# Performance work log

Hardware: AMD Instinct MI355X
Metric: run time of the kernel (lower is better)

The kernel has to match this reference:

```python
import jax, jax.numpy as jnp
import numpy as np


def _gcs_conv(x, a, w1, w2, b):
    # GCSConv: relu(A @ x W1 + x W2 + b);  x:[B,N,F], a:[B,N,N]
    return jax.nn.relu(jnp.einsum('bij,bjh->bih', a, x @ w1) + x @ w2 + b)


def _topk_pool(x, a, p, ratio=0.5):
    # score y = x . p/||p||, keep top ceil(ratio*N) nodes per graph,
    # gate kept node features with sigmoid(y), slice adjacency rows+cols.
    y = x @ (p / jnp.linalg.norm(p))            # [B, N]
    k = int(np.ceil(ratio * y.shape[1]))
    yk, idx = jax.lax.top_k(y, k)               # [B, k]
    xk = jnp.take_along_axis(x, idx[:, :, None], axis=1)
    xk = xk * jax.nn.sigmoid(yk)[:, :, None]    # gated node features [B,k,H]
    ak = jnp.take_along_axis(a, idx[:, :, None], axis=1)
    ak = jnp.take_along_axis(ak, idx[:, None, :], axis=2)  # [B,k,k]
    return xk, ak


def setup_inputs() -> dict:
    B, N, F0, H, C = 256, 512, 128, 32, 16
    key = jax.random.key(0)
    ks = jax.random.split(key, 12)
    s = lambda fan: 1.0 / np.sqrt(fan)
    return {
        'x': jax.random.normal(ks[0], (B, N, F0), jnp.float32),
        'a': jax.random.uniform(ks[1], (B, N, N), jnp.float32),
        'w1_1': jax.random.normal(ks[2], (F0, H), jnp.float32) * s(F0),
        'w2_1': jax.random.normal(ks[3], (F0, H), jnp.float32) * s(F0),
        'b1': jnp.zeros((H,), jnp.float32),
        'w1_2': jax.random.normal(ks[4], (H, H), jnp.float32) * s(H),
        'w2_2': jax.random.normal(ks[5], (H, H), jnp.float32) * s(H),
        'b2': jnp.zeros((H,), jnp.float32),
        'w1_3': jax.random.normal(ks[6], (H, H), jnp.float32) * s(H),
        'w2_3': jax.random.normal(ks[7], (H, H), jnp.float32) * s(H),
        'b3': jnp.zeros((H,), jnp.float32),
        'p_pool': jax.random.normal(ks[8], (H,), jnp.float32),
        'wd': jax.random.normal(ks[9], (H, C), jnp.float32) * s(H),
        'bd': jnp.zeros((C,), jnp.float32),
    }


def reference(x, a, w1_1, w2_1, b1, w1_2, w2_2, b2, w1_3, w2_3, b3, p_pool, wd, bd):
    x = _gcs_conv(x, a, w1_1, w2_1, b1)
    # NOTE: original code reuses pool1 twice -> shared p_pool for both stages
    x1, a1 = _topk_pool(x, a, p_pool)
    x1 = _gcs_conv(x1, a1, w1_2, w2_2, b2)
    x2, a2 = _topk_pool(x1, a1, p_pool)
    x2 = _gcs_conv(x2, a2, w1_3, w2_3, b3)
    pooled = jnp.mean(x2, axis=1)               # GlobalAvgPool over nodes [B,H]
    return jax.nn.softmax(pooled @ wd + bd, axis=-1)
```

## Files before the change

kernel.cpp:

```cpp
#include <hip/hip_runtime.h>
#include <cmath>

#define B 256
#define N0 512
#define F0 128
#define H 32
#define NC 16

template<int F, int RPT, int NPB, bool SCATTER>
__global__ __launch_bounds__(256) void k_xw(
    const float* __restrict__ x, const float* __restrict__ w1,
    const float* __restrict__ w2, const float* __restrict__ bias,
    const int* __restrict__ sidx,
    float* __restrict__ h, float* __restrict__ g) {
  __shared__ float w1t[H][F + 4];
  __shared__ float w2t[H][F + 4];
  __shared__ float bs[H];
  const int tid = threadIdx.x;
  for (int i = tid; i < F * H; i += 256) {
    int f = i >> 5, hc = i & 31;
    w1t[hc][f] = w1[i];
    w2t[hc][f] = w2[i];
  }
  if (tid < H) bs[tid] = bias[tid];
  __syncthreads();
  const int hq = tid & 7;
  const int rq = tid >> 3;
  const size_t row0 = (size_t)blockIdx.x * (32 * RPT) + (size_t)rq * RPT;
  const float* xb = x + row0 * F;
  float acc1[RPT][4];
  float acc2[RPT][4];
  #pragma unroll
  for (int r = 0; r < RPT; ++r)
    for (int c = 0; c < 4; ++c) { acc1[r][c] = 0.f; acc2[r][c] = 0.f; }
  for (int f0 = 0; f0 < F; f0 += 4) {
    float4 w1v[4], w2v[4];
    #pragma unroll
    for (int hh = 0; hh < 4; ++hh) {
      w1v[hh] = *(const float4*)&w1t[hq * 4 + hh][f0];
      w2v[hh] = *(const float4*)&w2t[hq * 4 + hh][f0];
    }
    #pragma unroll
    for (int r = 0; r < RPT; ++r) {
      float4 xv = *(const float4*)(xb + (size_t)r * F + f0);
      #pragma unroll
      for (int hh = 0; hh < 4; ++hh) {
        acc1[r][hh] += xv.x * w1v[hh].x + xv.y * w1v[hh].y + xv.z * w1v[hh].z + xv.w * w1v[hh].w;
        acc2[r][hh] += xv.x * w2v[hh].x + xv.y * w2v[hh].y + xv.z * w2v[hh].z + xv.w * w2v[hh].w;
      }
    }
  }
  #pragma unroll
  for (int r = 0; r < RPT; ++r) {
    size_t row = row0 + r;
    size_t go = row * H + hq * 4;
    size_t ho;
    if (SCATTER) {
      int b = (int)(row / NPB);
      int gid = sidx[row];
      ho = ((size_t)b * N0 + gid) * H + hq * 4;
    } else {
      ho = go;
    }
    float4 hv = make_float4(acc1[r][0], acc1[r][1], acc1[r][2], acc1[r][3]);
    float4 gv = make_float4(acc2[r][0] + bs[hq * 4 + 0], acc2[r][1] + bs[hq * 4 + 1],
                            acc2[r][2] + bs[hq * 4 + 2], acc2[r][3] + bs[hq * 4 + 3]);
    *(float4*)(h + ho) = hv;
    *(float4*)(g + go) = gv;
  }
}

template<int NROW, int RPT>
__global__ __launch_bounds__(256) void k_amm(
    const float* __restrict__ a0, const int* __restrict__ rid,
    const float* __restrict__ hf, const float* __restrict__ gbuf,
    float* __restrict__ out) {
  constexpr int RB = 32 * RPT;
  constexpr int JC = 64;
  constexpr int AS = JC + 2;
  __shared__ float atile[RB][AS];
  __shared__ float htile[JC][H];
  __shared__ int rowid[RB];
  const int tid = threadIdx.x;
  const int b = blockIdx.x;
  const int row0 = blockIdx.y * RB;
  for (int i = tid; i < RB; i += 256) {
    int row = row0 + i;
    rowid[i] = rid ? rid[(size_t)b * NROW + row] : row;
  }
  __syncthreads();
  const int hq = tid & 7;
  const int rq = tid >> 3;
  const float* abase = a0 + (size_t)b * N0 * N0;
  float acc[RPT][4];
  #pragma unroll
  for (int r = 0; r < RPT; ++r) { acc[r][0] = acc[r][1] = acc[r][2] = acc[r][3] = 0.f; }
  for (int j0 = 0; j0 < N0; j0 += JC) {
    if (j0) __syncthreads();
    {
      const float4* src = (const float4*)(hf + ((size_t)b * N0 + j0) * H);
      float4* dst = (float4*)htile;
      #pragma unroll
      for (int i = 0; i < JC * H / 4 / 256; ++i) dst[tid + i * 256] = src[tid + i * 256];
    }
    #pragma unroll
    for (int i = 0; i < RB * 16 / 256; ++i) {
      int c = tid + i * 256;
      int r = c >> 4, jc = c & 15;
      float4 v = *(const float4*)(abase + (size_t)rowid[r] * N0 + j0 + jc * 4);
      *(float2*)&atile[r][jc * 4] = make_float2(v.x, v.y);
      *(float2*)&atile[r][jc * 4 + 2] = make_float2(v.z, v.w);
    }
    __syncthreads();
    #pragma unroll 4
    for (int j = 0; j < JC; j += 4) {
      float4 hv[4];
      #pragma unroll
      for (int jj = 0; jj < 4; ++jj) hv[jj] = *(const float4*)&htile[j + jj][hq * 4];
      #pragma unroll
      for (int r = 0; r < RPT; ++r) {
        float2 a01 = *(const float2*)&atile[rq * RPT + r][j];
        float2 a23 = *(const float2*)&atile[rq * RPT + r][j + 2];
        acc[r][0] += a01.x * hv[0].x + a01.y * hv[1].x + a23.x * hv[2].x + a23.y * hv[3].x;
        acc[r][1] += a01.x * hv[0].y + a01.y * hv[1].y + a23.x * hv[2].y + a23.y * hv[3].y;
        acc[r][2] += a01.x * hv[0].z + a01.y * hv[1].z + a23.x * hv[2].z + a23.y * hv[3].z;
        acc[r][3] += a01.x * hv[0].w + a01.y * hv[1].w + a23.x * hv[2].w + a23.y * hv[3].w;
      }
    }
  }
  #pragma unroll
  for (int r = 0; r < RPT; ++r) {
    int row = row0 + rq * RPT + r;
    size_t o = ((size_t)b * NROW + row) * H + hq * 4;
    float4 gv = *(const float4*)(gbuf + o);
    float4 ov = make_float4(fmaxf(acc[r][0] + gv.x, 0.f), fmaxf(acc[r][1] + gv.y, 0.f),
                            fmaxf(acc[r][2] + gv.z, 0.f), fmaxf(acc[r][3] + gv.w, 0.f));
    *(float4*)(out + o) = ov;
  }
}

__global__ __launch_bounds__(256) void k_zero(float4* __restrict__ p, int n4) {
  int i = blockIdx.x * 256 + threadIdx.x;
  if (i < n4) p[i] = make_float4(0.f, 0.f, 0.f, 0.f);
}

template<int NN, int K>
__global__ __launch_bounds__(256) void k_topk(
    const float* __restrict__ x, const float* __restrict__ p,
    const int* __restrict__ prev_idx,
    float* __restrict__ xg, int* __restrict__ out_idx) {
  __shared__ float ys[NN];
  __shared__ int is[NN];
  __shared__ float ps[H];
  __shared__ float pns;
  const int tid = threadIdx.x;
  const int b = blockIdx.x;
  if (tid < H) ps[tid] = p[tid];
  __syncthreads();
  if (tid == 0) {
    float s = 0.f;
    for (int i = 0; i < H; ++i) s += ps[i] * ps[i];
    pns = 1.f / sqrtf(s);
  }
  __syncthreads();
  for (int i = tid; i < NN; i += 256) {
    const float* xr = x + ((size_t)b * NN + i) * H;
    float s = 0.f;
    #pragma unroll
    for (int f = 0; f < H; ++f) s += xr[f] * ps[f];
    ys[i] = s * pns;
    is[i] = i;
  }
  for (int k = 2; k <= NN; k <<= 1) {
    for (int j = k >> 1; j > 0; j >>= 1) {
      __syncthreads();
      for (int i = tid; i < NN; i += 256) {
        int ixj = i ^ j;
        if (ixj > i) {
          float v0 = ys[i], v1 = ys[ixj];
          int i0 = is[i], i1 = is[ixj];
          bool pre = (v1 > v0) || (v1 == v0 && i1 < i0);
          bool doswap = ((i & k) == 0) ? pre : !pre;
          if (doswap) { ys[i] = v1; ys[ixj] = v0; is[i] = i1; is[ixj] = i0; }
        }
      }
    }
  }
  for (int k = 2; k <= K; k <<= 1) {
    for (int j = k >> 1; j > 0; j >>= 1) {
      __syncthreads();
      for (int i = tid; i < K; i += 256) {
        int ixj = i ^ j;
        if (ixj > i && ixj < K) {
          float v0 = ys[i], v1 = ys[ixj];
          int i0 = is[i], i1 = is[ixj];
          bool pre = (i1 < i0);
          bool doswap = ((i & k) == 0) ? pre : !pre;
          if (doswap) { ys[i] = v1; ys[ixj] = v0; is[i] = i1; is[ixj] = i0; }
        }
      }
    }
  }
  __syncthreads();
  for (int t = tid; t < K * H; t += 256) {
    int kk = t >> 5, f = t & 31;
    int loc = is[kk];
    float gate = 1.f / (1.f + expf(-ys[kk]));
    xg[((size_t)b * K + kk) * H + f] = x[((size_t)b * NN + loc) * H + f] * gate;
  }
  for (int t = tid; t < K; t += 256)
    out_idx[(size_t)b * K + t] = prev_idx ? prev_idx[(size_t)b * NN + is[t]] : is[t];
}

__global__ __launch_bounds__(128) void k_head(
    const float* __restrict__ xl3, const float* __restrict__ wd,
    const float* __restrict__ bd, float* __restrict__ out) {
  __shared__ float part[4][H];
  __shared__ float pooled[H];
  __shared__ float wds[H * NC];
  __shared__ float logits[NC];
  const int tid = threadIdx.x;
  const int b = blockIdx.x;
  for (int i = tid; i < H * NC; i += 128) wds[i] = wd[i];
  const int f = tid & 31, nq = tid >> 5;
  float s = 0.f;
  for (int n = nq * 32; n < nq * 32 + 32; ++n)
    s += xl3[((size_t)b * 128 + n) * H + f];
  part[nq][f] = s;
  __syncthreads();
  if (tid < H)
    pooled[tid] = (part[0][tid] + part[1][tid] + part[2][tid] + part[3][tid]) * (1.f / 128.f);
  __syncthreads();
  if (tid < NC) {
    float acc = bd[tid];
    for (int i = 0; i < H; ++i) acc += pooled[i] * wds[i * NC + tid];
    logits[tid] = acc;
  }
  __syncthreads();
  if (tid == 0) {
    float mx = logits[0];
    for (int i = 1; i < NC; ++i) mx = fmaxf(mx, logits[i]);
    float e[NC], se = 0.f;
    for (int i = 0; i < NC; ++i) { e[i] = expf(logits[i] - mx); se += e[i]; }
    float inv = 1.f / se;
    for (int i = 0; i < NC; ++i) out[(size_t)b * NC + i] = e[i] * inv;
  }
}

extern "C" void kernel_launch(void* const* d_in, const int* in_sizes, int n_in,
                              void* d_out, int out_size, void* d_ws, size_t ws_size,
                              hipStream_t stream) {
  (void)in_sizes; (void)n_in; (void)out_size; (void)ws_size;
  const float* x    = (const float*)d_in[0];
  const float* a    = (const float*)d_in[1];
  const float* w1_1 = (const float*)d_in[2];
  const float* w2_1 = (const float*)d_in[3];
  const float* b1   = (const float*)d_in[4];
  const float* w1_2 = (const float*)d_in[5];
  const float* w2_2 = (const float*)d_in[6];
  const float* b2   = (const float*)d_in[7];
  const float* w1_3 = (const float*)d_in[8];
  const float* w2_3 = (const float*)d_in[9];
  const float* b3   = (const float*)d_in[10];
  const float* pp   = (const float*)d_in[11];
  const float* wd   = (const float*)d_in[12];
  const float* bd   = (const float*)d_in[13];
  float* out = (float*)d_out;

  char* w = (char*)d_ws;
  auto take = [&](size_t bytes) { char* r = w; w += (bytes + 255) & ~(size_t)255; return r; };
  float* h1  = (float*)take((size_t)B * N0 * H * 4);
  float* g1  = (float*)take((size_t)B * N0 * H * 4);
  float* xl1 = (float*)take((size_t)B * N0 * H * 4);
  int*   id1 = (int*)  take((size_t)B * 256 * 4);
  float* xg1 = (float*)take((size_t)B * 256 * H * 4);
  float* g2  = (float*)take((size_t)B * 256 * H * 4);
  float* xl2 = (float*)take((size_t)B * 256 * H * 4);
  int*   id2 = (int*)  take((size_t)B * 128 * 4);
  float* xg2 = (float*)take((size_t)B * 128 * H * 4);
  float* g3  = (float*)take((size_t)B * 128 * H * 4);
  float* xl3 = (float*)take((size_t)B * 128 * H * 4);
  float* hf2 = h1;
  float* hf3 = g1;

  k_xw<F0, 4, N0, false><<<dim3(B * N0 / 128), dim3(256), 0, stream>>>(
      x, w1_1, w2_1, b1, nullptr, h1, g1);
  k_amm<512, 4><<<dim3(B, 4), dim3(256), 0, stream>>>(a, nullptr, h1, g1, xl1);
  k_zero<<<dim3(2 * B * N0 * H / 4 / 256), dim3(256), 0, stream>>>(
      (float4*)h1, 2 * B * N0 * H / 4);
  k_topk<512, 256><<<dim3(B), dim3(256), 0, stream>>>(xl1, pp, nullptr, xg1, id1);
  k_xw<H, 4, 256, true><<<dim3(B * 256 / 128), dim3(256), 0, stream>>>(
      xg1, w1_2, w2_2, b2, id1, hf2, g2);
  k_amm<256, 2><<<dim3(B, 4), dim3(256), 0, stream>>>(a, id1, hf2, g2, xl2);
  k_topk<256, 128><<<dim3(B), dim3(256), 0, stream>>>(xl2, pp, id1, xg2, id2);
  k_xw<H, 4, 128, true><<<dim3(B * 128 / 128), dim3(256), 0, stream>>>(
      xg2, w1_3, w2_3, b3, id2, hf3, g3);
  k_amm<128, 1><<<dim3(B, 4), dim3(256), 0, stream>>>(a, id2, hf3, g3, xl3);
  k_head<<<dim3(B), dim3(128), 0, stream>>>(xl3, wd, bd, out);
}
```

Baseline: 639.2 us.

## Register-prefetch next adjacency and feature tiles in A-matmul kernel

The adjacency matmul kernel now loads the next JC-column chunk of the gathered adjacency rows and node features into registers while the current chunk is being computed from shared memory. The goal is to hide global-memory latency behind the FMAs. The shared tile padding changes from +2 to +4, so each row can be written and read as a single float4 instead of two float2 accesses. In exchange the kernel uses more registers for the prefetch buffers, which may lower occupancy.

```diff
diff --git a/kernel.cpp b/kernel.cpp
--- a/kernel.cpp
+++ b/kernel.cpp
@@ -77,7 +77,9 @@
     float* __restrict__ out) {
   constexpr int RB = 32 * RPT;
   constexpr int JC = 64;
-  constexpr int AS = JC + 2;
+  constexpr int AS = JC + 4;
+  constexpr int AI = RB / 16;
+  constexpr int HI = JC * H / 4 / 256;
   __shared__ float atile[RB][AS];
   __shared__ float htile[JC][H];
   __shared__ int rowid[RB];
@@ -91,42 +93,49 @@
   __syncthreads();
   const int hq = tid & 7;
   const int rq = tid >> 3;
+  const int ar = tid >> 4;
+  const int ac = tid & 15;
   const float* abase = a0 + (size_t)b * N0 * N0;
+  const float4* hsrc = (const float4*)(hf + (size_t)b * N0 * H);
+  float4 abuf[AI], hbuf[HI];
+  #pragma unroll
+  for (int i = 0; i < AI; ++i)
+    abuf[i] = *(const float4*)(abase + (size_t)rowid[ar + i * 16] * N0 + ac * 4);
+  #pragma unroll
+  for (int i = 0; i < HI; ++i) hbuf[i] = hsrc[tid + i * 256];
   float acc[RPT][4];
   #pragma unroll
   for (int r = 0; r < RPT; ++r) { acc[r][0] = acc[r][1] = acc[r][2] = acc[r][3] = 0.f; }
-  for (int j0 = 0; j0 < N0; j0 += JC) {
-    if (j0) __syncthreads();
-    {
-      const float4* src = (const float4*)(hf + ((size_t)b * N0 + j0) * H);
-      float4* dst = (float4*)htile;
-      #pragma unroll
-      for (int i = 0; i < JC * H / 4 / 256; ++i) dst[tid + i * 256] = src[tid + i * 256];
-    }
-    #pragma unroll
-    for (int i = 0; i < RB * 16 / 256; ++i) {
-      int c = tid + i * 256;
-      int r = c >> 4, jc = c & 15;
-      float4 v = *(const float4*)(abase + (size_t)rowid[r] * N0 + j0 + jc * 4);
-      *(float2*)&atile[r][jc * 4] = make_float2(v.x, v.y);
-      *(float2*)&atile[r][jc * 4 + 2] = make_float2(v.z, v.w);
-    }
+  for (int c = 0; c < N0 / JC; ++c) {
+    #pragma unroll
+    for (int i = 0; i < AI; ++i)
+      *(float4*)&atile[ar + i * 16][ac * 4] = abuf[i];
+    #pragma unroll
+    for (int i = 0; i < HI; ++i) ((float4*)htile)[tid + i * 256] = hbuf[i];
     __syncthreads();
-    #pragma unroll 4
+    if (c + 1 < N0 / JC) {
+      const int j0 = (c + 1) * JC;
+      #pragma unroll
+      for (int i = 0; i < AI; ++i)
+        abuf[i] = *(const float4*)(abase + (size_t)rowid[ar + i * 16] * N0 + j0 + ac * 4);
+      #pragma unroll
+      for (int i = 0; i < HI; ++i) hbuf[i] = hsrc[j0 * (H / 4) + tid + i * 256];
+    }
+    #pragma unroll
     for (int j = 0; j < JC; j += 4) {
       float4 hv[4];
       #pragma unroll
       for (int jj = 0; jj < 4; ++jj) hv[jj] = *(const float4*)&htile[j + jj][hq * 4];
       #pragma unroll
       for (int r = 0; r < RPT; ++r) {
-        float2 a01 = *(const float2*)&atile[rq * RPT + r][j];
-        float2 a23 = *(const float2*)&atile[rq * RPT + r][j + 2];
-        acc[r][0] += a01.x * hv[0].x + a01.y * hv[1].x + a23.x * hv[2].x + a23.y * hv[3].x;
-        acc[r][1] += a01.x * hv[0].y + a01.y * hv[1].y + a23.x * hv[2].y + a23.y * hv[3].y;
-        acc[r][2] += a01.x * hv[0].z + a01.y * hv[1].z + a23.x * hv[2].z + a23.y * hv[3].z;
-        acc[r][3] += a01.x * hv[0].w + a01.y * hv[1].w + a23.x * hv[2].w + a23.y * hv[3].w;
+        float4 av = *(const float4*)&atile[rq * RPT + r][j];
+        acc[r][0] += av.x * hv[0].x + av.y * hv[1].x + av.z * hv[2].x + av.w * hv[3].x;
+        acc[r][1] += av.x * hv[0].y + av.y * hv[1].y + av.z * hv[2].y + av.w * hv[3].y;
+        acc[r][2] += av.x * hv[0].z + av.y * hv[1].z + av.z * hv[2].z + av.w * hv[3].z;
+        acc[r][3] += av.x * hv[0].w + av.y * hv[1].w + av.z * hv[2].w + av.w * hv[3].w;
       }
     }
+    __syncthreads();
   }
   #pragma unroll
   for (int r = 0; r < RPT; ++r) {
```

After: 744.8 us. 1.17x slower.

## Use split-bf16 MFMA for adjacency matmuls with transposed hi/lo feature buffers

Applied to the files above, without the earlier changes.

The FP32 scalar A@H kernels are replaced by MFMA 16x16x32 bf16 kernels. Both the adjacency and the features are split into bf16 hi and lo parts, and three products are accumulated to keep near-fp32 accuracy. New transpose kernels write the features in a K-major bf16 layout, scattered to global node ids for the pooled stages. This removes the FP32 FMA-bound inner loop, but it adds per-tile conversion of A, extra transpose and zeroing passes, and some precision loss from dropping the lo*lo term.

```diff
diff --git a/kernel.cpp b/kernel.cpp
--- a/kernel.cpp
+++ b/kernel.cpp
@@ -7,11 +7,20 @@
 #define H 32
 #define NC 16
 
-template<int F, int RPT, int NPB, bool SCATTER>
+typedef short v8s __attribute__((ext_vector_type(8)));
+typedef float v4f __attribute__((ext_vector_type(4)));
+
+__device__ inline ushort bf16_rne(float f) {
+  unsigned u = __float_as_uint(f);
+  unsigned r = (u + 0x7FFF + ((u >> 16) & 1)) >> 16;
+  return (ushort)r;
+}
+__device__ inline float bf16_f(ushort s) { return __uint_as_float((unsigned)s << 16); }
+
+template<int F, int RPT>
 __global__ __launch_bounds__(256) void k_xw(
     const float* __restrict__ x, const float* __restrict__ w1,
     const float* __restrict__ w2, const float* __restrict__ bias,
-    const int* __restrict__ sidx,
     float* __restrict__ h, float* __restrict__ g) {
   __shared__ float w1t[H][F + 4];
   __shared__ float w2t[H][F + 4];
@@ -52,90 +61,138 @@
   }
   #pragma unroll
   for (int r = 0; r < RPT; ++r) {
-    size_t row = row0 + r;
-    size_t go = row * H + hq * 4;
-    size_t ho;
-    if (SCATTER) {
-      int b = (int)(row / NPB);
-      int gid = sidx[row];
-      ho = ((size_t)b * N0 + gid) * H + hq * 4;
-    } else {
-      ho = go;
-    }
+    size_t o = (row0 + r) * H + hq * 4;
     float4 hv = make_float4(acc1[r][0], acc1[r][1], acc1[r][2], acc1[r][3]);
     float4 gv = make_float4(acc2[r][0] + bs[hq * 4 + 0], acc2[r][1] + bs[hq * 4 + 1],
                             acc2[r][2] + bs[hq * 4 + 2], acc2[r][3] + bs[hq * 4 + 3]);
-    *(float4*)(h + ho) = hv;
-    *(float4*)(g + go) = gv;
-  }
-}
-
-template<int NROW, int RPT>
-__global__ __launch_bounds__(256) void k_amm(
+    *(float4*)(h + o) = hv;
+    *(float4*)(g + o) = gv;
+  }
+}
+
+__global__ __launch_bounds__(256) void k_trans_d(
+    const float* __restrict__ hsrc, ushort* __restrict__ hTh, ushort* __restrict__ hTl) {
+  __shared__ ushort thi[H][72];
+  __shared__ ushort tlo[H][72];
+  const int tid = threadIdx.x;
+  const int b = blockIdx.x;
+  const int jr = tid >> 2, kq = tid & 3;
+  const int hh = tid >> 3, seg = tid & 7;
+  for (int j0 = 0; j0 < N0; j0 += 64) {
+    if (j0) __syncthreads();
+    const float* src = hsrc + (((size_t)b * N0) + j0 + jr) * H + kq * 8;
+    float4 v0 = *(const float4*)src;
+    float4 v1 = *(const float4*)(src + 4);
+    float vv[8] = {v0.x, v0.y, v0.z, v0.w, v1.x, v1.y, v1.z, v1.w};
+    #pragma unroll
+    for (int i = 0; i < 8; ++i) {
+      ushort hi = bf16_rne(vv[i]);
+      thi[kq * 8 + i][jr] = hi;
+      tlo[kq * 8 + i][jr] = bf16_rne(vv[i] - bf16_f(hi));
+    }
+    __syncthreads();
+    size_t o = ((size_t)b * H + hh) * N0 + j0 + seg * 8;
+    *(uint4*)&hTh[o] = *(const uint4*)&thi[hh][seg * 8];
+    *(uint4*)&hTl[o] = *(const uint4*)&tlo[hh][seg * 8];
+  }
+}
+
+template<int K>
+__global__ __launch_bounds__(256) void k_trans_s(
+    const float* __restrict__ hd, const int* __restrict__ idx,
+    ushort* __restrict__ hTh, ushort* __restrict__ hTl) {
+  const int tid = threadIdx.x;
+  const int b = blockIdx.x;
+  for (int t = tid; t < K * 4; t += 256) {
+    int row = t >> 2, kq = t & 3;
+    int gid = idx[(size_t)b * K + row];
+    const float* src = hd + (((size_t)b * K) + row) * H + kq * 8;
+    float4 v0 = *(const float4*)src;
+    float4 v1 = *(const float4*)(src + 4);
+    float vv[8] = {v0.x, v0.y, v0.z, v0.w, v1.x, v1.y, v1.z, v1.w};
+    #pragma unroll
+    for (int i = 0; i < 8; ++i) {
+      ushort hi = bf16_rne(vv[i]);
+      size_t o = ((size_t)b * H + kq * 8 + i) * N0 + gid;
+      hTh[o] = hi;
+      hTl[o] = bf16_rne(vv[i] - bf16_f(hi));
+    }
+  }
+}
+
+template<int NROW>
+__global__ __launch_bounds__(256) void k_ammx(
     const float* __restrict__ a0, const int* __restrict__ rid,
-    const float* __restrict__ hf, const float* __restrict__ gbuf,
-    float* __restrict__ out) {
-  constexpr int RB = 32 * RPT;
-  constexpr int JC = 64;
-  constexpr int AS = JC + 2;
-  __shared__ float atile[RB][AS];
-  __shared__ float htile[JC][H];
+    const ushort* __restrict__ hTh, const ushort* __restrict__ hTl,
+    const float* __restrict__ g, float* __restrict__ out) {
+  constexpr int RB = 64;
+  constexpr int KC = 32;
+  constexpr int ASP = KC + 8;
+  __shared__ ushort ah[RB][ASP];
+  __shared__ ushort al[RB][ASP];
+  __shared__ ushort bh[H][ASP];
+  __shared__ ushort bl[H][ASP];
   __shared__ int rowid[RB];
   const int tid = threadIdx.x;
   const int b = blockIdx.x;
   const int row0 = blockIdx.y * RB;
-  for (int i = tid; i < RB; i += 256) {
-    int row = row0 + i;
-    rowid[i] = rid ? rid[(size_t)b * NROW + row] : row;
-  }
-  __syncthreads();
-  const int hq = tid & 7;
-  const int rq = tid >> 3;
+  if (tid < RB) rowid[tid] = rid ? rid[(size_t)b * NROW + row0 + tid] : row0 + tid;
+  __syncthreads();
+  const int wave = tid >> 6, lane = tid & 63;
+  const int m = lane & 15, quad = lane >> 4;
+  const int sr = tid >> 2, skq = tid & 3;
+  const int shh = tid >> 3, sseg = tid & 7;
   const float* abase = a0 + (size_t)b * N0 * N0;
-  float acc[RPT][4];
+  const ushort* bhsrc = hTh + ((size_t)b * H + shh) * N0 + sseg * 4;
+  const ushort* blsrc = hTl + ((size_t)b * H + shh) * N0 + sseg * 4;
+  v4f acc0 = {0.f, 0.f, 0.f, 0.f};
+  v4f acc1 = {0.f, 0.f, 0.f, 0.f};
+  for (int k0 = 0; k0 < N0; k0 += KC) {
+    if (k0) __syncthreads();
+    {
+      const float* ap = abase + (size_t)rowid[sr] * N0 + k0 + skq * 4;
+      float4 v0 = *(const float4*)ap;
+      float4 v1 = *(const float4*)(ap + 16);
+      ushort4 h0, l0, h1, l1;
+      h0.x = bf16_rne(v0.x); l0.x = bf16_rne(v0.x - bf16_f(h0.x));
+      h0.y = bf16_rne(v0.y); l0.y = bf16_rne(v0.y - bf16_f(h0.y));
+      h0.z = bf16_rne(v0.z); l0.z = bf16_rne(v0.z - bf16_f(h0.z));
+      h0.w = bf16_rne(v0.w); l0.w = bf16_rne(v0.w - bf16_f(h0.w));
+      h1.x = bf16_rne(v1.x); l1.x = bf16_rne(v1.x - bf16_f(h1.x));
+      h1.y = bf16_rne(v1.y); l1.y = bf16_rne(v1.y - bf16_f(h1.y));
+      h1.z = bf16_rne(v1.z); l1.z = bf16_rne(v1.z - bf16_f(h1.z));
+      h1.w = bf16_rne(v1.w); l1.w = bf16_rne(v1.w - bf16_f(h1.w));
+      *(ushort4*)&ah[sr][skq * 4] = h0;      *(ushort4*)&al[sr][skq * 4] = l0;
+      *(ushort4*)&ah[sr][skq * 4 + 16] = h1; *(ushort4*)&al[sr][skq * 4 + 16] = l1;
+    }
+    {
+      *(ushort4*)&bh[shh][sseg * 4] = *(const ushort4*)(bhsrc + k0);
+      *(ushort4*)&bl[shh][sseg * 4] = *(const ushort4*)(blsrc + k0);
+    }
+    __syncthreads();
+    const int arow = wave * 16 + m;
+    v8s Ah = *(const v8s*)&ah[arow][quad * 8];
+    v8s Al = *(const v8s*)&al[arow][quad * 8];
+    v8s Bh0 = *(const v8s*)&bh[m][quad * 8];
+    v8s Bh1 = *(const v8s*)&bh[16 + m][quad * 8];
+    v8s Bl0 = *(const v8s*)&bl[m][quad * 8];
+    v8s Bl1 = *(const v8s*)&bl[16 + m][quad * 8];
+    acc0 = __builtin_amdgcn_mfma_f32_16x16x32_bf16(Ah, Bh0, acc0, 0, 0, 0);
+    acc1 = __builtin_amdgcn_mfma_f32_16x16x32_bf16(Ah, Bh1, acc1, 0, 0, 0);
+    acc0 = __builtin_amdgcn_mfma_f32_16x16x32_bf16(Al, Bh0, acc0, 0, 0, 0);
+    acc1 = __builtin_amdgcn_mfma_f32_16x16x32_bf16(Al, Bh1, acc1, 0, 0, 0);
+    acc0 = __builtin_amdgcn_mfma_f32_16x16x32_bf16(Ah, Bl0, acc0, 0, 0, 0);
+    acc1 = __builtin_amdgcn_mfma_f32_16x16x32_bf16(Ah, Bl1, acc1, 0, 0, 0);
+  }
   #pragma unroll
-  for (int r = 0; r < RPT; ++r) { acc[r][0] = acc[r][1] = acc[r][2] = acc[r][3] = 0.f; }
-  for (int j0 = 0; j0 < N0; j0 += JC) {
-    if (j0) __syncthreads();
-    {
-      const float4* src = (const float4*)(hf + ((size_t)b * N0 + j0) * H);
-      float4* dst = (float4*)htile;
-      #pragma unroll
-      for (int i = 0; i < JC * H / 4 / 256; ++i) dst[tid + i * 256] = src[tid + i * 256];
-    }
-    #pragma unroll
-    for (int i = 0; i < RB * 16 / 256; ++i) {
-      int c = tid + i * 256;
-      int r = c >> 4, jc = c & 15;
-      float4 v = *(const float4*)(abase + (size_t)rowid[r] * N0 + j0 + jc * 4);
-      *(float2*)&atile[r][jc * 4] = make_float2(v.x, v.y);
-      *(float2*)&atile[r][jc * 4 + 2] = make_float2(v.z, v.w);
-    }
-    __syncthreads();
-    #pragma unroll 4
-    for (int j = 0; j < JC; j += 4) {
-      float4 hv[4];
-      #pragma unroll
-      for (int jj = 0; jj < 4; ++jj) hv[jj] = *(const float4*)&htile[j + jj][hq * 4];
-      #pragma unroll
-      for (int r = 0; r < RPT; ++r) {
-        float2 a01 = *(const float2*)&atile[rq * RPT + r][j];
-        float2 a23 = *(const float2*)&atile[rq * RPT + r][j + 2];
-        acc[r][0] += a01.x * hv[0].x + a01.y * hv[1].x + a23.x * hv[2].x + a23.y * hv[3].x;
-        acc[r][1] += a01.x * hv[0].y + a01.y * hv[1].y + a23.x * hv[2].y + a23.y * hv[3].y;
-        acc[r][2] += a01.x * hv[0].z + a01.y * hv[1].z + a23.x * hv[2].z + a23.y * hv[3].z;
-        acc[r][3] += a01.x * hv[0].w + a01.y * hv[1].w + a23.x * hv[2].w + a23.y * hv[3].w;
-      }
-    }
-  }
-  #pragma unroll
-  for (int r = 0; r < RPT; ++r) {
-    int row = row0 + rq * RPT + r;
-    size_t o = ((size_t)b * NROW + row) * H + hq * 4;
-    float4 gv = *(const float4*)(gbuf + o);
-    float4 ov = make_float4(fmaxf(acc[r][0] + gv.x, 0.f), fmaxf(acc[r][1] + gv.y, 0.f),
-                            fmaxf(acc[r][2] + gv.z, 0.f), fmaxf(acc[r][3] + gv.w, 0.f));
-    *(float4*)(out + o) = ov;
+  for (int reg = 0; reg < 4; ++reg) {
+    int row = row0 + wave * 16 + quad * 4 + reg;
+    size_t o0 = ((size_t)b * NROW + row) * H + m;
+    size_t o1 = o0 + 16;
+    float v0 = acc0[reg] + g[o0];
+    float v1 = acc1[reg] + g[o1];
+    out[o0] = fmaxf(v0, 0.f);
+    out[o1] = fmaxf(v1, 0.f);
   }
 }
 
@@ -269,32 +326,35 @@
 
   char* w = (char*)d_ws;
   auto take = [&](size_t bytes) { char* r = w; w += (bytes + 255) & ~(size_t)255; return r; };
-  float* h1  = (float*)take((size_t)B * N0 * H * 4);
-  float* g1  = (float*)take((size_t)B * N0 * H * 4);
-  float* xl1 = (float*)take((size_t)B * N0 * H * 4);
-  int*   id1 = (int*)  take((size_t)B * 256 * 4);
-  float* xg1 = (float*)take((size_t)B * 256 * H * 4);
-  float* g2  = (float*)take((size_t)B * 256 * H * 4);
-  float* xl2 = (float*)take((size_t)B * 256 * H * 4);
-  int*   id2 = (int*)  take((size_t)B * 128 * 4);
-  float* xg2 = (float*)take((size_t)B * 128 * H * 4);
-  float* g3  = (float*)take((size_t)B * 128 * H * 4);
-  float* xl3 = (float*)take((size_t)B * 128 * H * 4);
-  float* hf2 = h1;
-  float* hf3 = g1;
-
-  k_xw<F0, 4, N0, false><<<dim3(B * N0 / 128), dim3(256), 0, stream>>>(
-      x, w1_1, w2_1, b1, nullptr, h1, g1);
-  k_amm<512, 4><<<dim3(B, 4), dim3(256), 0, stream>>>(a, nullptr, h1, g1, xl1);
-  k_zero<<<dim3(2 * B * N0 * H / 4 / 256), dim3(256), 0, stream>>>(
-      (float4*)h1, 2 * B * N0 * H / 4);
+  float*  h1  = (float*) take((size_t)B * N0 * H * 4);
+  float*  g1  = (float*) take((size_t)B * N0 * H * 4);
+  ushort* hTh = (ushort*)take((size_t)B * H * N0 * 2);
+  ushort* hTl = (ushort*)take((size_t)B * H * N0 * 2);
+  float*  xl1 = (float*) take((size_t)B * N0 * H * 4);
+  int*    id1 = (int*)   take((size_t)B * 256 * 4);
+  float*  xg1 = (float*) take((size_t)B * 256 * H * 4);
+  float*  h2  = (float*) take((size_t)B * 256 * H * 4);
+  float*  g2  = (float*) take((size_t)B * 256 * H * 4);
+  float*  xl2 = (float*) take((size_t)B * 256 * H * 4);
+  int*    id2 = (int*)   take((size_t)B * 128 * 4);
+  float*  xg2 = (float*) take((size_t)B * 128 * H * 4);
+  float*  h3  = (float*) take((size_t)B * 128 * H * 4);
+  float*  g3  = (float*) take((size_t)B * 128 * H * 4);
+  float*  xl3 = (float*) take((size_t)B * 128 * H * 4);
+  const int hT4 = (int)((size_t)B * H * N0 * 2 * 2 / 16);
+
+  k_xw<F0, 2><<<dim3(B * N0 / 64), dim3(256), 0, stream>>>(x, w1_1, w2_1, b1, h1, g1);
+  k_trans_d<<<dim3(B), dim3(256), 0, stream>>>(h1, hTh, hTl);
+  k_ammx<512><<<dim3(B, 8), dim3(256), 0, stream>>>(a, nullptr, hTh, hTl, g1, xl1);
   k_topk<512, 256><<<dim3(B), dim3(256), 0, stream>>>(xl1, pp, nullptr, xg1, id1);
-  k_xw<H, 4, 256, true><<<dim3(B * 256 / 128), dim3(256), 0, stream>>>(
-      xg1, w1_2, w2_2, b2, id1, hf2, g2);
-  k_amm<256, 2><<<dim3(B, 4), dim3(256), 0, stream>>>(a, id1, hf2, g2, xl2);
+  k_xw<H, 4><<<dim3(B * 256 / 128), dim3(256), 0, stream>>>(xg1, w1_2, w2_2, b2, h2, g2);
+  k_zero<<<dim3((hT4 + 255) / 256), dim3(256), 0, stream>>>((float4*)hTh, hT4);
+  k_trans_s<256><<<dim3(B), dim3(256), 0, stream>>>(h2, id1, hTh, hTl);
+  k_ammx<256><<<dim3(B, 4), dim3(256), 0, stream>>>(a, id1, hTh, hTl, g2, xl2);
   k_topk<256, 128><<<dim3(B), dim3(256), 0, stream>>>(xl2, pp, id1, xg2, id2);
-  k_xw<H, 4, 128, true><<<dim3(B * 128 / 128), dim3(256), 0, stream>>>(
-      xg2, w1_3, w2_3, b3, id2, hf3, g3);
-  k_amm<128, 1><<<dim3(B, 4), dim3(256), 0, stream>>>(a, id2, hf3, g3, xl3);
+  k_xw<H, 4><<<dim3(B * 128 / 128), dim3(256), 0, stream>>>(xg2, w1_3, w2_3, b3, h3, g3);
+  k_zero<<<dim3((hT4 + 255) / 256), dim3(256), 0, stream>>>((float4*)hTh, hT4);
+  k_trans_s<128><<<dim3(B), dim3(256), 0, stream>>>(h3, id2, hTh, hTl);
+  k_ammx<128><<<dim3(B, 2), dim3(256), 0, stream>>>(a, id2, hTh, hTl, g3, xl3);
   k_head<<<dim3(B), dim3(128), 0, stream>>>(xl3, wd, bd, out);
 }
```

Result: faster. 602.2 us (-5.8%).
